# Optimization experiments

Hardware: AMD Instinct MI355X
Metric: run time of the kernel (lower is better)

## Reference

```python
import jax, jax.numpy as jnp
import numpy as np

M, K, N = 8192, 4096, 4096
DIV = 1.0 / (127.0 * 127.0)


def setup_inputs() -> dict:
    key = jax.random.key(0)
    k1, k2, k3, k4, k5 = jax.random.split(key, 5)
    x = jax.random.randint(k1, (M, K), -127, 128, dtype=jnp.int8)
    weight_int8 = jax.random.randint(k2, (N, K), -127, 128, dtype=jnp.int8)
    scale_x = jnp.abs(jax.random.normal(k3, (M,), dtype=jnp.float32)) * 0.01
    scale_w = jnp.abs(jax.random.normal(k4, (N,), dtype=jnp.float32)) * 0.01
    bias = (jax.random.normal(k5, (N,), dtype=jnp.float32) * 0.01).astype(jnp.float16)
    return {"x": x, "scale_x": scale_x, "weight_int8": weight_int8,
            "scale_w": scale_w, "bias": bias}


def reference(x, scale_x, weight_int8, scale_w, bias):
    # int8 GEMM with int32 accumulation: [M,K] @ [K,N]
    acc = jax.lax.dot_general(
        x, weight_int8.T,
        dimension_numbers=(((1,), (0,)), ((), ())),
        preferred_element_type=jnp.int32,
    ).astype(jnp.float32)
    # fused rowwise/colwise dequant + bias, cast to fp16
    out = acc * DIV * scale_x[:, None] * scale_w[None, :] + bias.astype(jnp.float32)[None, :]
    return out.astype(jnp.float16)
```

## Files before the change

### kernel.cpp

```cpp
#include <hip/hip_runtime.h>
#include <hip/hip_fp16.h>
#include <cstdint>
#include <cstddef>

#define M_DIM 8192
#define N_DIM 4096
#define K_DIM 4096

typedef int v4i __attribute__((ext_vector_type(4)));

__global__ __launch_bounds__(256) void pack_i32_to_i8(const int* __restrict__ srcX,
                                                      uint32_t* __restrict__ dstX,
                                                      const int* __restrict__ srcW,
                                                      uint32_t* __restrict__ dstW,
                                                      int nx4, int ntot) {
    int i = blockIdx.x * 256 + threadIdx.x;
    if (i >= ntot) return;
    const int* s;
    uint32_t*  d;
    int j;
    if (i < nx4) { s = srcX; d = dstX; j = i; }
    else         { s = srcW; d = dstW; j = i - nx4; }
    int4 a = ((const int4*)s)[j];
#if __has_builtin(__builtin_amdgcn_perm)
    uint32_t lo = __builtin_amdgcn_perm((uint32_t)a.y, (uint32_t)a.x, 0x0400);
    uint32_t hi = __builtin_amdgcn_perm((uint32_t)a.w, (uint32_t)a.z, 0x0400);
    d[j] = __builtin_amdgcn_perm(hi, lo, 0x05040100);
#else
    d[j] = (uint32_t)(a.x & 0xff) | ((uint32_t)(a.y & 0xff) << 8) |
           ((uint32_t)(a.z & 0xff) << 16) | ((uint32_t)a.w << 24);
#endif
}

__device__ __forceinline__ void gload_lds16(const int8_t* g, int8_t* l) {
    __builtin_amdgcn_global_load_lds(
        (const __attribute__((address_space(1))) void*)g,
        (__attribute__((address_space(3))) void*)l, 16, 0, 0);
}


#define VMW(n) asm volatile("s_waitcnt vmcnt(" #n ")" ::: "memory")

#define LOADF(DA, DB, DC, KT1)                                                \
    do {                                                                      \
        const int8_t* _b = lds + ((KT1) & 3) * 32768;                         \
        _Pragma("unroll")                                                     \
        for (int i = 0; i < 4; ++i) {                                         \
            DA[i] = *(const v4i*)(_b + aoff + i * 1024);                      \
            DB[i] = *(const v4i*)(_b + 16384 + boff + i * 1024);              \
            DC[i] = *(const v4i*)(_b + aoff + 4096 + i * 1024);               \
        }                                                                     \
    } while (0)

#define STAGE(KT3)                                                            \
    do {                                                                      \
        int8_t* _s = lds + ((KT3) & 3) * 32768;                               \
        gload_lds16(gA0 + (KT3) * 64, _s + ldsoff);                           \
        gload_lds16(gA1 + (KT3) * 64, _s + ldsoff + 8192);                    \
        gload_lds16(gB0 + (KT3) * 64, _s + 16384 + ldsoff);                   \
        gload_lds16(gB1 + (KT3) * 64, _s + 16384 + ldsoff + 8192);            \
    } while (0)

#define MFMA32(CA, CB, CC)                                                    \
    __builtin_amdgcn_s_setprio(1);                                            \
    _Pragma("unroll")                                                         \
    for (int mi = 0; mi < 4; ++mi) {                                          \
        _Pragma("unroll")                                                     \
        for (int ni = 0; ni < 4; ++ni)                                        \
            acc[mi][ni] = __builtin_amdgcn_mfma_i32_16x16x64_i8(              \
                CA[mi], CB[ni], acc[mi][ni], 0, 0, 0);                        \
    }                                                                         \
    _Pragma("unroll")                                                         \
    for (int mi = 0; mi < 4; ++mi) {                                          \
        _Pragma("unroll")                                                     \
        for (int ni = 0; ni < 4; ++ni)                                        \
            acc[4 + mi][ni] = __builtin_amdgcn_mfma_i32_16x16x64_i8(          \
                CC[mi], CB[ni], acc[4 + mi][ni], 0, 0, 0);                    \
    }                                                                         \
    __builtin_amdgcn_s_setprio(0);

#define ITER(KT, CA, CB, CC, NA, NB, NC, DOREAD, DOSTAGE, VMSTMT, DOSYNC)     \
    do {                                                                      \
        if (DOREAD) LOADF(NA, NB, NC, (KT) + 1);                              \
        if (DOSTAGE) STAGE((KT) + 3);                                         \
        __builtin_amdgcn_sched_barrier(0);       \
        MFMA32(CA, CB, CC);                                                   \
        if (DOSYNC) {                                                         \
            __builtin_amdgcn_sched_barrier(0);                                \
            VMSTMT;                                                           \
            __builtin_amdgcn_s_barrier();                                     \
            __builtin_amdgcn_sched_barrier(0);                                \
        }                                                                     \
    } while (0)

__global__ __launch_bounds__(512, 2) void gemm_i8_dq(const int8_t* __restrict__ A,
                                                     const int8_t* __restrict__ W,
                                                     const float* __restrict__ sx,
                                                     const float* __restrict__ sw,
                                                     const float* __restrict__ bias,
                                                     float* __restrict__ out) {
    __shared__ __attribute__((aligned(16))) int8_t lds[131072];

    const int t    = threadIdx.x;
    const int lane = t & 63;
    const int w    = t >> 6;
    const int wm   = w >> 2;
    const int wn   = w & 3;

    const int flat = blockIdx.y * 16 + blockIdx.x;
    const int xcd  = flat & 7;
    const int idx  = flat >> 3;
    const int bm   = (xcd >> 1) * 8 + (idx & 7);
    const int bn   = (xcd & 1) * 8 + (idx >> 3);

    const int srow   = t >> 2;
    const int rot    = (srow >> 1) & 3;
    const int gchunk = ((t & 3) + rot) & 3;
    const int scol   = gchunk * 16;
    const int8_t* gA0 = A + (size_t)(bm * 256 + srow) * K_DIM + scol;
    const int8_t* gA1 = gA0 + (size_t)128 * K_DIM;
    const int8_t* gB0 = W + (size_t)(bn * 256 + srow) * K_DIM + scol;
    const int8_t* gB1 = gB0 + (size_t)128 * K_DIM;
    const int ldsoff = t * 16;

    const int rho  = lane & 15;
    const int p16  = (((lane >> 4) - (rho >> 1)) & 3) * 16;
    const int aoff = (wm * 128 + rho) * 64 + p16;
    const int boff = (wn * 64 + rho) * 64 + p16;

    v4i acc[8][4];
    const v4i vzero = {0, 0, 0, 0};
#pragma unroll
    for (int mi = 0; mi < 8; mi++)
#pragma unroll
        for (int ni = 0; ni < 4; ni++) acc[mi][ni] = vzero;

    v4i pA[4], pB[4], pC[4], qA[4], qB[4], qC[4];

#pragma unroll
    for (int pt = 0; pt < 3; ++pt) {
        int8_t* bufA = lds + pt * 32768;
        gload_lds16(gA0 + pt * 64, bufA + ldsoff);
        gload_lds16(gA1 + pt * 64, bufA + ldsoff + 8192);
        gload_lds16(gB0 + pt * 64, bufA + 16384 + ldsoff);
        gload_lds16(gB1 + pt * 64, bufA + 16384 + ldsoff + 8192);
    }
    VMW(4);
    __builtin_amdgcn_s_barrier();
    __builtin_amdgcn_sched_barrier(0);
    LOADF(pA, pB, pC, 0);

    for (int kt = 0; kt < 60; kt += 2) {
        ITER(kt,     pA, pB, pC, qA, qB, qC, true, true, VMW(4), true);
        ITER(kt + 1, qA, qB, qC, pA, pB, pC, true, true, VMW(4), true);
    }
    ITER(60, pA, pB, pC, qA, qB, qC, true,  true,  VMW(4),  true);
    ITER(61, qA, qB, qC, pA, pB, pC, true,  false, VMW(0),  true);
    ITER(62, pA, pB, pC, qA, qB, qC, true,  false, ((void)0), false);
    ITER(63, qA, qB, qC, pA, pB, pC, false, false, ((void)0), false);

    const float DIVF = (float)(1.0 / (127.0 * 127.0));
    const int col0 = bn * 256 + wn * 64 + (lane & 15);
    const int row0 = bm * 256 + wm * 128 + (lane >> 4) * 4;

    float swv[4], bv[4];
#pragma unroll
    for (int ni = 0; ni < 4; ni++) {
        swv[ni] = sw[col0 + ni * 16];
        bv[ni]  = bias[col0 + ni * 16];
    }

#pragma unroll
    for (int mi = 0; mi < 8; mi++) {
#pragma unroll
        for (int r = 0; r < 4; r++) {
            const int row = row0 + mi * 16 + r;
            const float xs = sx[row];
#pragma unroll
            for (int ni = 0; ni < 4; ni++) {
                float v = __fmul_rn((float)acc[mi][ni][r], DIVF);
                v = __fmul_rn(v, xs);
                v = __fmul_rn(v, swv[ni]);
                v = __fadd_rn(v, bv[ni]);
                out[(size_t)row * N_DIM + col0 + ni * 16] = __half2float(__float2half(v));
            }
        }
    }
}

extern "C" void kernel_launch(void* const* d_in, const int* in_sizes, int n_in,
                              void* d_out, int out_size, void* d_ws, size_t ws_size,
                              hipStream_t stream) {
    const int*   x_i32 = (const int*)d_in[0];
    const float* sx    = (const float*)d_in[1];
    const int*   w_i32 = (const int*)d_in[2];
    const float* sw    = (const float*)d_in[3];
    const float* bias  = (const float*)d_in[4];
    float* out = (float*)d_out;

    uint8_t* xb = (uint8_t*)d_ws;
    uint8_t* wb = (uint8_t*)d_ws + (size_t)M_DIM * K_DIM;

    const int nx4  = (M_DIM * K_DIM) / 4;
    const int nw4  = (N_DIM * K_DIM) / 4;
    const int ntot = nx4 + nw4;
    pack_i32_to_i8<<<(ntot + 255) / 256, 256, 0, stream>>>(
        x_i32, (uint32_t*)xb, w_i32, (uint32_t*)wb, nx4, ntot);

    dim3 grid(N_DIM / 256, M_DIM / 256);
    gemm_i8_dq<<<grid, 512, 0, stream>>>((const int8_t*)xb, (const int8_t*)wb,
                                         sx, sw, bias, out);
}
```

Measured before the change: 383.8 us.

## Load B operand directly from global into registers, bypassing LDS

The weight (B) tile is no longer staged through LDS. Each wave now reads its own 64-column slice of W straight into registers, one k-step ahead, while only the A tile stays in the 4-deep LDS ring. This halves LDS use per block, which could allow two resident blocks per CU, and removes the B LDS writes and reads. In exchange, B is fetched redundantly by the two wm waves, and its global load latency is hidden by only a single iteration of MFMA work, with the vmcnt waits adjusted to match.

```diff
diff --git a/kernel.cpp b/kernel.cpp
--- a/kernel.cpp
+++ b/kernel.cpp
@@ -41,24 +41,28 @@
 
 #define VMW(n) asm volatile("s_waitcnt vmcnt(" #n ")" ::: "memory")
 
-#define LOADF(DA, DB, DC, KT1)                                                \
-    do {                                                                      \
-        const int8_t* _b = lds + ((KT1) & 3) * 32768;                         \
+#define LOADFA(DA, DC, KT1)                                                   \
+    do {                                                                      \
+        const int8_t* _b = lds + ((KT1) & 3) * 16384;                         \
         _Pragma("unroll")                                                     \
         for (int i = 0; i < 4; ++i) {                                         \
             DA[i] = *(const v4i*)(_b + aoff + i * 1024);                      \
-            DB[i] = *(const v4i*)(_b + 16384 + boff + i * 1024);              \
             DC[i] = *(const v4i*)(_b + aoff + 4096 + i * 1024);               \
         }                                                                     \
     } while (0)
 
-#define STAGE(KT3)                                                            \
-    do {                                                                      \
-        int8_t* _s = lds + ((KT3) & 3) * 32768;                               \
+#define LOADB(DB, KT1)                                                        \
+    do {                                                                      \
+        _Pragma("unroll")                                                     \
+        for (int i = 0; i < 4; ++i)                                           \
+            DB[i] = *(const v4i*)(gBL + (size_t)i * (16 * K_DIM) + (KT1) * 64); \
+    } while (0)
+
+#define STAGEA(KT3)                                                           \
+    do {                                                                      \
+        int8_t* _s = lds + ((KT3) & 3) * 16384;                               \
         gload_lds16(gA0 + (KT3) * 64, _s + ldsoff);                           \
         gload_lds16(gA1 + (KT3) * 64, _s + ldsoff + 8192);                    \
-        gload_lds16(gB0 + (KT3) * 64, _s + 16384 + ldsoff);                   \
-        gload_lds16(gB1 + (KT3) * 64, _s + 16384 + ldsoff + 8192);            \
     } while (0)
 
 #define MFMA32(CA, CB, CC)                                                    \
@@ -81,9 +85,12 @@
 
 #define ITER(KT, CA, CB, CC, NA, NB, NC, DOREAD, DOSTAGE, VMSTMT, DOSYNC)     \
     do {                                                                      \
-        if (DOREAD) LOADF(NA, NB, NC, (KT) + 1);                              \
-        if (DOSTAGE) STAGE((KT) + 3);                                         \
-        __builtin_amdgcn_sched_barrier(0);       \
+        if (DOREAD) {                                                         \
+            LOADB(NB, (KT) + 1);                                              \
+            LOADFA(NA, NC, (KT) + 1);                                         \
+        }                                                                     \
+        if (DOSTAGE) STAGEA((KT) + 3);                                        \
+        __builtin_amdgcn_sched_barrier(0);                                    \
         MFMA32(CA, CB, CC);                                                   \
         if (DOSYNC) {                                                         \
             __builtin_amdgcn_sched_barrier(0);                                \
@@ -99,7 +106,7 @@
                                                      const float* __restrict__ sw,
                                                      const float* __restrict__ bias,
                                                      float* __restrict__ out) {
-    __shared__ __attribute__((aligned(16))) int8_t lds[131072];
+    __shared__ __attribute__((aligned(16))) int8_t lds[65536];
 
     const int t    = threadIdx.x;
     const int lane = t & 63;
@@ -119,14 +126,14 @@
     const int scol   = gchunk * 16;
     const int8_t* gA0 = A + (size_t)(bm * 256 + srow) * K_DIM + scol;
     const int8_t* gA1 = gA0 + (size_t)128 * K_DIM;
-    const int8_t* gB0 = W + (size_t)(bn * 256 + srow) * K_DIM + scol;
-    const int8_t* gB1 = gB0 + (size_t)128 * K_DIM;
     const int ldsoff = t * 16;
 
     const int rho  = lane & 15;
     const int p16  = (((lane >> 4) - (rho >> 1)) & 3) * 16;
     const int aoff = (wm * 128 + rho) * 64 + p16;
-    const int boff = (wn * 64 + rho) * 64 + p16;
+
+    const int8_t* gBL = W + (size_t)(bn * 256 + wn * 64 + (lane & 15)) * K_DIM
+                          + ((lane >> 4) * 16);
 
     v4i acc[8][4];
     const v4i vzero = {0, 0, 0, 0};
@@ -139,23 +146,23 @@
 
 #pragma unroll
     for (int pt = 0; pt < 3; ++pt) {
-        int8_t* bufA = lds + pt * 32768;
+        int8_t* bufA = lds + pt * 16384;
         gload_lds16(gA0 + pt * 64, bufA + ldsoff);
         gload_lds16(gA1 + pt * 64, bufA + ldsoff + 8192);
-        gload_lds16(gB0 + pt * 64, bufA + 16384 + ldsoff);
-        gload_lds16(gB1 + pt * 64, bufA + 16384 + ldsoff + 8192);
-    }
-    VMW(4);
+    }
+    LOADB(pB, 0);
+    __builtin_amdgcn_sched_barrier(0);
+    VMW(6);
     __builtin_amdgcn_s_barrier();
     __builtin_amdgcn_sched_barrier(0);
-    LOADF(pA, pB, pC, 0);
+    LOADFA(pA, pC, 0);
 
     for (int kt = 0; kt < 60; kt += 2) {
-        ITER(kt,     pA, pB, pC, qA, qB, qC, true, true, VMW(4), true);
-        ITER(kt + 1, qA, qB, qC, pA, pB, pC, true, true, VMW(4), true);
-    }
-    ITER(60, pA, pB, pC, qA, qB, qC, true,  true,  VMW(4),  true);
-    ITER(61, qA, qB, qC, pA, pB, pC, true,  false, VMW(0),  true);
+        ITER(kt,     pA, pB, pC, qA, qB, qC, true, true, VMW(6), true);
+        ITER(kt + 1, qA, qB, qC, pA, pB, pC, true, true, VMW(6), true);
+    }
+    ITER(60, pA, pB, pC, qA, qB, qC, true,  true,  VMW(6),    true);
+    ITER(61, qA, qB, qC, pA, pB, pC, true,  false, VMW(4),    true);
     ITER(62, pA, pB, pC, qA, qB, qC, true,  false, ((void)0), false);
     ITER(63, qA, qB, qC, pA, pB, pC, false, false, ((void)0), false);
 
```

Result: slower. 442.3 us (+15.2%).
